# Performance work log

Measured on AMD Instinct MI355X. Metric: run time of the kernel, lower is better.

The kernel has to match this reference:

```python
import jax, jax.numpy as jnp
import numpy as np

B, T, E, H = 2, 2048, 1024, 4
Dk = E // H          # 256 head qk dim
Dv = Dk * 2          # 512 head v dim (expansion_ratio=2)
EPS = 1e-5
ROPE_BASE = 10000.0


def setup_inputs() -> dict:
    key = jax.random.key(0)
    ks = jax.random.split(key, 7)
    s = 0.02  # small init matching xavier gains in reset_parameters
    return {
        "x": jax.random.normal(ks[0], (B, T, E), jnp.float32),
        "Wq": jax.random.normal(ks[1], (E, E), jnp.float32) * s,
        "Wk": jax.random.normal(ks[2], (E, E), jnp.float32) * s,
        "Wv": jax.random.normal(ks[3], (E, 2 * E), jnp.float32) * s,
        "Wg": jax.random.normal(ks[4], (E, 2 * E), jnp.float32) * s,
        "Wo": jax.random.normal(ks[5], (2 * E, E), jnp.float32) * s,
        "gn_weight": jnp.ones((Dv,), jnp.float32),
    }


def _rotary(q, k):
    # q,k: [b, t, h, d]; non-interleaved (GPT-NeoX) rotary over the full head dim
    d = q.shape[-1]
    inv_freq = 1.0 / (ROPE_BASE ** (jnp.arange(0, d, 2, dtype=jnp.float32) / d))
    t = jnp.arange(q.shape[1], dtype=jnp.float32)
    freqs = jnp.einsum('t,f->tf', t, inv_freq)      # [t, d/2]
    cos = jnp.cos(freqs)[None, :, None, :]
    sin = jnp.sin(freqs)[None, :, None, :]

    def rot(x):
        x1, x2 = x[..., : d // 2], x[..., d // 2:]
        return jnp.concatenate([x1 * cos - x2 * sin, x2 * cos + x1 * sin], axis=-1)

    return rot(q), rot(k)


def reference(x, Wq, Wk, Wv, Wg, Wo, gn_weight):
    b, t, e = x.shape
    q = (x @ Wq).reshape(b, t, H, Dk)
    k = (x @ Wk).reshape(b, t, H, Dk)
    q, k = _rotary(q, k)
    q = q.transpose(0, 2, 1, 3) * (Dk ** -0.5)      # [b,h,t,dk], scale = head_qk_dim^-0.5
    k = k.transpose(0, 2, 1, 3)
    v = (x @ Wv).reshape(b, t, H, Dv).transpose(0, 2, 1, 3)  # [b,h,t,dv]

    # RetNet per-head decay: gamma_h = 1 - 2^-(5+h)
    gamma = 1.0 - jnp.exp2(-5.0 - jnp.arange(H, dtype=jnp.float32))
    ti = jnp.arange(t)
    n = ti[:, None] - ti[None, :]                   # t - s
    decay = jnp.where(
        n >= 0,
        gamma[:, None, None] ** jnp.maximum(n, 0).astype(jnp.float32),
        0.0,
    )                                               # [h,t,t] causal decayed mask

    scores = jnp.einsum('bhtd,bhsd->bhts', q, k) * decay[None]
    o = jnp.einsum('bhts,bhsd->bhtd', scores, v)    # [b,h,t,dv]
    o = o.transpose(0, 2, 1, 3)                     # [b,t,h,dv]

    # per-head RMSNorm (group_norm over head_v_dim)
    rms = jnp.sqrt(jnp.mean(o * o, axis=-1, keepdims=True) + EPS)
    o = o / rms * gn_weight

    # NOTE: the given source multiplies by raw g_proj(x) (gate_fn not applied in forward)
    g = x @ Wg                                      # [b,t,2E]
    return (o.reshape(b, t, H * Dv) * g) @ Wo       # [b,t,E]
```

## Files before the change

kernel.cpp:

```cpp
#include <hip/hip_runtime.h>
#include <hip/hip_bf16.h>

#define B_ 2
#define T_ 2048
#define E_ 1024
#define DK 256
#define DV 512
#define MROWS 4096
#define LDQKVG 6144
#define CHK 128
#define NCHK 16

typedef __attribute__((ext_vector_type(8))) short short8;
typedef __attribute__((ext_vector_type(4))) short short4v;
typedef __attribute__((ext_vector_type(4))) float floatx4;

typedef __attribute__((address_space(3))) unsigned as3_u32;
typedef const __attribute__((address_space(1))) unsigned as1_u32;

static __device__ __forceinline__ void gld_lds16(const unsigned short* gsrc, unsigned short* ldst) {
  __builtin_amdgcn_global_load_lds((as1_u32*)gsrc, (as3_u32*)ldst, 16, 0, 0);
}

static __device__ __forceinline__ float bf2f(unsigned short u) {
  union { unsigned int i; float f; } x; x.i = ((unsigned int)u) << 16; return x.f;
}
static __device__ __forceinline__ unsigned short f2bf(float f) {
  __hip_bfloat16 h = __float2bfloat16(f);
  return __builtin_bit_cast(unsigned short, h);
}

__global__ void __launch_bounds__(256) prep_kernel(
    const float* __restrict__ x, unsigned short* __restrict__ xb,
    const float* __restrict__ Wq, const float* __restrict__ Wk,
    const float* __restrict__ Wv, const float* __restrict__ Wg,
    unsigned short* __restrict__ WallT,
    const float* __restrict__ Wo, unsigned short* __restrict__ WoT,
    float2* __restrict__ ropetab) {
  __shared__ float tile[32][33];
  int bid = blockIdx.x;
  int tid = threadIdx.x;
  if (bid < 2048) {
    int i = bid * 256 + tid;
    size_t base = (size_t)i * 8;
    float4 a = *(const float4*)(x + base);
    float4 b = *(const float4*)(x + base + 4);
    short8 o;
    o[0] = (short)f2bf(a.x); o[1] = (short)f2bf(a.y);
    o[2] = (short)f2bf(a.z); o[3] = (short)f2bf(a.w);
    o[4] = (short)f2bf(b.x); o[5] = (short)f2bf(b.y);
    o[6] = (short)f2bf(b.z); o[7] = (short)f2bf(b.w);
    *(short8*)(xb + base) = o;
    return;
  }
  if (bid < 8192) {
    bid -= 2048;
    const float* in; unsigned short* o; int ldin, nbx;
    if (bid < 1024)      { in = Wq; o = WallT;                       ldin = 1024; nbx = 32; }
    else if (bid < 2048) { in = Wk; o = WallT + (size_t)1024 * 1024; ldin = 1024; nbx = 32; bid -= 1024; }
    else if (bid < 4096) { in = Wv; o = WallT + (size_t)2048 * 1024; ldin = 2048; nbx = 64; bid -= 2048; }
    else                 { in = Wg; o = WallT + (size_t)4096 * 1024; ldin = 2048; nbx = 64; bid -= 4096; }
    int c0 = (bid % nbx) * 32, r0 = (bid / nbx) * 32;
    int tx = tid & 31, ty = tid >> 5;
#pragma unroll
    for (int i = 0; i < 32; i += 8)
      tile[ty + i][tx] = in[(size_t)(r0 + ty + i) * ldin + c0 + tx];
    __syncthreads();
#pragma unroll
    for (int i = 0; i < 32; i += 8)
      o[(size_t)(c0 + ty + i) * 1024 + r0 + tx] = f2bf(tile[tx][ty + i]);
    return;
  }
  if (bid < 9216) {
    int idx = (bid - 8192) * 256 + tid;
    int t = idx >> 7, j = idx & 127;
    float invf = exp2f(-(float)j * (13.287712379549449f / 128.0f));
    float ang = (float)t * invf;
    ropetab[idx] = make_float2(cosf(ang), sinf(ang));
    return;
  }
  {
    int lb = bid - 9216;
    int c0 = (lb & 31) * 32, r0 = (lb >> 5) * 32;
    int tx = tid & 31, ty = tid >> 5;
#pragma unroll
    for (int i = 0; i < 32; i += 8)
      tile[ty + i][tx] = Wo[(size_t)(r0 + ty + i) * 1024 + c0 + tx];
    __syncthreads();
#pragma unroll
    for (int i = 0; i < 32; i += 8)
      WoT[(size_t)(c0 + ty + i) * 2048 + r0 + tx] = f2bf(tile[tx][ty + i]);
  }
}

template<int BM, int BN, int WM_W, int WN_W, int MINW, bool F32OUT>
__global__ void __launch_bounds__(WM_W * WN_W * 64, MINW) gemmp_kernel(
    const unsigned short* __restrict__ A, int lda,
    const unsigned short* __restrict__ Bt, int ldb, int K,
    void* __restrict__ Cp, int ldc, int ccol0, int nbx) {
  constexpr int WAVES = WM_W * WN_W;
  constexpr int AG = BM / 16 / WAVES;
  constexpr int BG = BN / 16 / WAVES;
  constexpr int RM = BM / WM_W;
  constexpr int CN = BN / WN_W;
  constexpr int MB = RM / 16, NB = CN / 16;
  __shared__ __align__(16) unsigned short lds[3][(BM + BN) * 32];
  const int tid = threadIdx.x;
  const int lane = tid & 63;
  const int wid = tid >> 6;
  const int wm = wid / WN_W, wn = wid % WN_W;
  const int bid = blockIdx.x;
  const int m0 = (bid % nbx) * BM;
  const int n0 = (bid / nbx) * BN;
  const unsigned short* Ab = A + (size_t)m0 * lda;
  const unsigned short* Bb = Bt + (size_t)n0 * ldb;
  const int NT = K / 32;

  auto stage = [&](int sl, int t) {
    const int k0 = t * 32;
#pragma unroll
    for (int j = 0; j < AG; ++j) {
      int g = wid * AG + j;
      int ci = g * 64 + lane;
      int row = ci >> 2, c = ci & 3;
      int cs = c ^ ((row >> 1) & 3);
      gld_lds16(Ab + (size_t)row * lda + k0 + cs * 8, &lds[sl][g * 512]);
    }
#pragma unroll
    for (int j = 0; j < BG; ++j) {
      int g = wid * BG + j;
      int ci = g * 64 + lane;
      int row = ci >> 2, c = ci & 3;
      int cs = c ^ ((row >> 1) & 3);
      gld_lds16(Bb + (size_t)row * ldb + k0 + cs * 8, &lds[sl][BM * 32 + g * 512]);
    }
  };

  floatx4 acc[MB][NB];
#pragma unroll
  for (int i = 0; i < MB; i++)
#pragma unroll
    for (int j = 0; j < NB; j++)
      acc[i][j] = (floatx4){0.f, 0.f, 0.f, 0.f};

  stage(0, 0);
  stage(1, 1);

  int cur = 0;
#pragma unroll 1
  for (int t = 0; t < NT; ++t) {
    if (t + 1 < NT) {
      if constexpr (AG + BG == 2) asm volatile("s_waitcnt vmcnt(2)" ::: "memory");
      else if constexpr (AG + BG == 3) asm volatile("s_waitcnt vmcnt(3)" ::: "memory");
      else if constexpr (AG + BG == 4) asm volatile("s_waitcnt vmcnt(4)" ::: "memory");
      else if constexpr (AG + BG == 6) asm volatile("s_waitcnt vmcnt(6)" ::: "memory");
      else asm volatile("s_waitcnt vmcnt(8)" ::: "memory");
    } else {
      asm volatile("s_waitcnt vmcnt(0)" ::: "memory");
    }
    __builtin_amdgcn_s_barrier();
    asm volatile("" ::: "memory");
    int sl = cur + 2; if (sl >= 3) sl -= 3;
    if (t + 2 < NT) stage(sl, t + 2);

    const unsigned short* As_ = lds[cur];
    const unsigned short* Bs_ = lds[cur] + BM * 32;
    short8 af[MB], bfv[NB];
#pragma unroll
    for (int i = 0; i < MB; ++i) {
      int row = wm * RM + i * 16 + (lane & 15);
      af[i] = *(const short8*)&As_[row * 32 + (((lane >> 4) ^ ((row >> 1) & 3)) * 8)];
    }
#pragma unroll
    for (int j = 0; j < NB; ++j) {
      int nn = wn * CN + j * 16 + (lane & 15);
      bfv[j] = *(const short8*)&Bs_[nn * 32 + (((lane >> 4) ^ ((nn >> 1) & 3)) * 8)];
    }
#pragma unroll
    for (int i = 0; i < MB; ++i)
#pragma unroll
      for (int j = 0; j < NB; ++j)
        acc[i][j] = __builtin_amdgcn_mfma_f32_16x16x32_bf16(af[i], bfv[j], acc[i][j], 0, 0, 0);
    cur = cur + 1 == 3 ? 0 : cur + 1;
  }

#pragma unroll
  for (int i = 0; i < MB; ++i)
#pragma unroll
    for (int j = 0; j < NB; ++j)
#pragma unroll
      for (int r = 0; r < 4; ++r) {
        int row = m0 + wm * RM + i * 16 + (lane >> 4) * 4 + r;
        int col = ccol0 + n0 + wn * CN + j * 16 + (lane & 15);
        float v = acc[i][j][r];
        if (F32OUT) ((float*)Cp)[(size_t)row * ldc + col] = v;
        else ((unsigned short*)Cp)[(size_t)row * ldc + col] = f2bf(v);
      }
}

__global__ void __launch_bounds__(256) postproc_kernel(
    unsigned short* __restrict__ qkvg, const float2* __restrict__ tab,
    unsigned short* __restrict__ kTs, unsigned short* __restrict__ vT) {
  __shared__ unsigned short kt[256][33];
  __shared__ unsigned short vt[512][33];
  const int tid = threadIdx.x;
  const int rt = blockIdx.x >> 2, h = blockIdx.x & 3;
  const int grow0 = rt * 32;
  const float lg = log2f(1.0f - exp2f(-5.0f - (float)h));
  const int r = tid >> 3;
  const int grow = grow0 + r;
  const int t = grow & (T_ - 1);
  const float sq = 0.0625f * exp2f((float)(t & (CHK - 1)) * lg);
  const float fac = exp2f((float)(CHK - (t & (CHK - 1))) * lg);
#pragma unroll
  for (int half = 0; half < 2; ++half) {
    int j0 = (tid & 7) * 8 + half * 64;
    size_t base = (size_t)grow * LDQKVG + h * DK + j0;
    short8 q1 = *(const short8*)&qkvg[base],      q2 = *(const short8*)&qkvg[base + 128];
    short8 k1 = *(const short8*)&qkvg[base + E_], k2 = *(const short8*)&qkvg[base + E_ + 128];
    short8 oq1, oq2, ok1, ok2;
#pragma unroll
    for (int e = 0; e < 8; ++e) {
      float2 cs = tab[(t << 7) + j0 + e];
      float c = cs.x, s = cs.y;
      float a1 = bf2f((unsigned short)q1[e]), a2 = bf2f((unsigned short)q2[e]);
      float b1 = bf2f((unsigned short)k1[e]), b2 = bf2f((unsigned short)k2[e]);
      float rk1 = b1 * c - b2 * s, rk2 = b2 * c + b1 * s;
      oq1[e] = (short)f2bf((a1 * c - a2 * s) * sq);
      oq2[e] = (short)f2bf((a2 * c + a1 * s) * sq);
      ok1[e] = (short)f2bf(rk1);
      ok2[e] = (short)f2bf(rk2);
      kt[j0 + e][r]       = f2bf(rk1 * fac);
      kt[j0 + e + 128][r] = f2bf(rk2 * fac);
    }
    *(short8*)&qkvg[base]            = oq1;
    *(short8*)&qkvg[base + 128]      = oq2;
    *(short8*)&qkvg[base + E_]       = ok1;
    *(short8*)&qkvg[base + E_ + 128] = ok2;
  }
  __syncthreads();
  {
    int dk = tid;
    unsigned short* dst = kTs + (size_t)(h * DK + dk) * MROWS + grow0;
#pragma unroll
    for (int i = 0; i < 4; ++i) {
      short8 w;
#pragma unroll
      for (int e = 0; e < 8; ++e) w[e] = (short)kt[dk][i * 8 + e];
      *(short8*)(dst + i * 8) = w;
    }
  }
  {
    int cv = tid & 7;
#pragma unroll
    for (int i = 0; i < 8; ++i) {
      int col = cv * 64 + i * 8;
      short8 v = *(const short8*)&qkvg[(size_t)grow * LDQKVG + 2048 + h * DV + col];
#pragma unroll
      for (int e = 0; e < 8; ++e) vt[col + e][r] = (unsigned short)v[e];
    }
  }
  __syncthreads();
#pragma unroll
  for (int p = 0; p < 2; ++p) {
    int dv = p * 256 + tid;
    unsigned short* dst = vT + (size_t)(h * DV + dv) * MROWS + grow0;
#pragma unroll
    for (int i = 0; i < 4; ++i) {
      short8 w;
#pragma unroll
      for (int e = 0; e < 8; ++e) w[e] = (short)vt[dv][i * 8 + e];
      *(short8*)(dst + i * 8) = w;
    }
  }
}

__global__ void __launch_bounds__(256) state_kernel(
    const unsigned short* __restrict__ kTs, const unsigned short* __restrict__ vT,
    unsigned short* __restrict__ Sbuf) {
  const int lane = threadIdx.x & 63, wid = threadIdx.x >> 6;
  const int bh = blockIdx.x & 7, dkt = (blockIdx.x >> 3) & 3, dvt = (blockIdx.x >> 5) & 15;
  const int b = bh >> 2, h = bh & 3;
  const float lg = log2f(1.0f - exp2f(-5.0f - (float)h));
  const float g128 = exp2f((float)CHK * lg);
  const int dk0 = dkt * 64 + wid * 16;
  const int dv0 = dvt * 32;
  const unsigned short* arow = kTs + (size_t)(h * DK + dk0 + (lane & 15)) * MROWS + b * T_ + (lane >> 4) * 8;
  const unsigned short* brow = vT + (size_t)(h * DV + dv0 + (lane & 15)) * MROWS + b * T_ + (lane >> 4) * 8;
  floatx4 acc[2];
  acc[0] = (floatx4){0.f, 0.f, 0.f, 0.f};
  acc[1] = (floatx4){0.f, 0.f, 0.f, 0.f};
#pragma unroll 4
  for (int c = 0; c < NCHK; ++c) {
    size_t sb = (size_t)(c * 8 + bh) * (DV * DK);
#pragma unroll
    for (int nb = 0; nb < 2; ++nb) {
      short4v o;
#pragma unroll
      for (int r = 0; r < 4; ++r) o[r] = (short)f2bf(acc[nb][r]);
      *(short4v*)&Sbuf[sb + (size_t)(dv0 + nb * 16 + (lane & 15)) * DK + dk0 + (lane >> 4) * 4] = o;
    }
#pragma unroll
    for (int nb = 0; nb < 2; ++nb)
#pragma unroll
      for (int r = 0; r < 4; ++r) acc[nb][r] *= g128;
#pragma unroll
    for (int ks = 0; ks < 4; ++ks) {
      short8 a = *(const short8*)(arow + c * CHK + ks * 32);
#pragma unroll
      for (int nb = 0; nb < 2; ++nb) {
        short8 bb = *(const short8*)(brow + (size_t)nb * 16 * MROWS + c * CHK + ks * 32);
        acc[nb] = __builtin_amdgcn_mfma_f32_16x16x32_bf16(a, bb, acc[nb], 0, 0, 0);
      }
    }
  }
}

__global__ void __launch_bounds__(256) retention3_kernel(
    const unsigned short* __restrict__ qkvg, const unsigned short* __restrict__ vT,
    const unsigned short* __restrict__ Sbuf, const float* __restrict__ gnw,
    unsigned short* __restrict__ og) {
  __shared__ unsigned short k_lds[32 * 256];
  __shared__ unsigned short v_lds[512 * 32];
  __shared__ unsigned short s_lds[4][16 * 40];
  const int tid = threadIdx.x, lane = tid & 63, wid = tid >> 6;
  const int bh  = blockIdx.x & 7;
  const int c   = (blockIdx.x >> 3) & 15;
  const int rhf = (blockIdx.x >> 7) & 1;
  const int b = bh >> 2, h = bh & 3;
  const float lg = log2f(1.0f - exp2f(-5.0f - (float)h));
  const int rb0 = b * T_ + c * CHK + rhf * 64;
  const int taub = rhf * 64 + wid * 16;
  const int nst = rhf ? 4 : 2;
  const unsigned short* kbase = qkvg + (size_t)(b * T_ + c * CHK) * LDQKVG + E_ + h * DK;
  const unsigned short* vbase = vT + (size_t)(h * DV) * MROWS + b * T_ + c * CHK;
  const unsigned short* Sp = Sbuf + (size_t)(c * 8 + bh) * (DV * DK);

  auto stage = [&](int st) {
    int s0 = st * 32;
#pragma unroll
    for (int j = 0; j < 4; ++j) {
      int ci = (wid * 4 + j) * 64 + lane;
      int row = ci >> 5, cc = ci & 31;
      int cs = cc ^ (row & 7);
      gld_lds16(kbase + (size_t)(s0 + row) * LDQKVG + cs * 8, &k_lds[(wid * 4 + j) * 512]);
    }
#pragma unroll
    for (int j = 0; j < 8; ++j) {
      int ci = (wid * 8 + j) * 64 + lane;
      int dv = ci >> 2, cc = ci & 3;
      int cs = cc ^ ((dv ^ (dv >> 2)) & 3);
      gld_lds16(vbase + (size_t)dv * MROWS + s0 + cs * 8, &v_lds[(wid * 8 + j) * 512]);
    }
  };

  stage(0);

  short8 qf[8];
  {
    int qrow = rb0 + wid * 16 + (lane & 15);
    const unsigned short* qp = qkvg + (size_t)qrow * LDQKVG + h * DK + (lane >> 4) * 8;
#pragma unroll
    for (int kk = 0; kk < 8; kk++) qf[kk] = *(const short8*)(qp + kk * 32);
  }
  floatx4 oacc[32];
#pragma unroll
  for (int nb = 0; nb < 32; ++nb) oacc[nb] = (floatx4){0.f, 0.f, 0.f, 0.f};
#pragma unroll
  for (int ks = 0; ks < 8; ++ks) {
#pragma unroll
    for (int nb = 0; nb < 32; ++nb) {
      short8 sf = *(const short8*)&Sp[(size_t)(nb * 16 + (lane & 15)) * DK + ks * 32 + (lane >> 4) * 8];
      oacc[nb] = __builtin_amdgcn_mfma_f32_16x16x32_bf16(qf[ks], sf, oacc[nb], 0, 0, 0);
    }
  }

#pragma unroll 1
  for (int st = 0; st < nst; ++st) {
    __syncthreads();
#pragma unroll
    for (int ch = 0; ch < 2; ++ch) {
      floatx4 f = (floatx4){0.f, 0.f, 0.f, 0.f};
      const int srow = ch * 16 + (lane & 15);
      __builtin_amdgcn_s_setprio(1);
#pragma unroll
      for (int kk = 0; kk < 8; kk++) {
        int cc = (kk * 4 + (lane >> 4)) ^ (srow & 7);
        short8 kf = *(const short8*)&k_lds[srow * 256 + cc * 8];
        f = __builtin_amdgcn_mfma_f32_16x16x32_bf16(qf[kk], kf, f, 0, 0, 0);
      }
      __builtin_amdgcn_s_setprio(0);
#pragma unroll
      for (int r = 0; r < 4; ++r) {
        int lr = (lane >> 4) * 4 + r;
        int sig = st * 32 + ch * 16 + (lane & 15);
        int n = taub + lr - sig;
        float val = (n >= 0) ? f[r] * exp2f(-(float)sig * lg) : 0.0f;
        s_lds[wid][lr * 40 + ch * 16 + (lane & 15)] = f2bf(val);
      }
    }
    short8 af = *(const short8*)&s_lds[wid][(lane & 15) * 40 + (lane >> 4) * 8];
    __builtin_amdgcn_s_setprio(1);
#pragma unroll
    for (int nb = 0; nb < 32; ++nb) {
      int dv = nb * 16 + (lane & 15);
      int cc = (lane >> 4) ^ ((dv ^ (dv >> 2)) & 3);
      short8 vf = *(const short8*)&v_lds[dv * 32 + cc * 8];
      oacc[nb] = __builtin_amdgcn_mfma_f32_16x16x32_bf16(af, vf, oacc[nb], 0, 0, 0);
    }
    __builtin_amdgcn_s_setprio(0);
    if (st + 1 < nst) {
      __syncthreads();
      stage(st + 1);
    }
  }
#pragma unroll
  for (int r = 0; r < 4; ++r) {
    float ss = 0.f;
#pragma unroll
    for (int nb = 0; nb < 32; nb++) { float xv = oacc[nb][r]; ss += xv * xv; }
    ss += __shfl_xor(ss, 1, 64);
    ss += __shfl_xor(ss, 2, 64);
    ss += __shfl_xor(ss, 4, 64);
    ss += __shfl_xor(ss, 8, 64);
    float inv = rsqrtf(ss * (1.0f / 512.0f) + 1e-5f);
    int row = rb0 + wid * 16 + (lane >> 4) * 4 + r;
    size_t growbase = (size_t)row * LDQKVG + 4096 + h * DV;
    size_t orowbase = (size_t)row * LDQKVG + h * DV;
#pragma unroll
    for (int nb = 0; nb < 32; nb++) {
      int col = nb * 16 + (lane & 15);
      float gv = bf2f(qkvg[growbase + col]);
      og[orowbase + col] = f2bf(oacc[nb][r] * inv * gnw[col] * gv);
    }
  }
}

extern "C" void kernel_launch(void* const* d_in, const int* in_sizes, int n_in,
                              void* d_out, int out_size, void* d_ws, size_t ws_size,
                              hipStream_t stream) {
  const float* x   = (const float*)d_in[0];
  const float* Wq  = (const float*)d_in[1];
  const float* Wk  = (const float*)d_in[2];
  const float* Wv  = (const float*)d_in[3];
  const float* Wg  = (const float*)d_in[4];
  const float* Wo  = (const float*)d_in[5];
  const float* gnw = (const float*)d_in[6];
  float* out = (float*)d_out;

  char* ws = (char*)d_ws;
  size_t off = 0;
  auto alloc = [&](size_t bytes) { char* p = ws + off; off += (bytes + 255) & ~(size_t)255; return p; };
  unsigned short* qkvg = (unsigned short*)alloc((size_t)MROWS * LDQKVG * 2);
  unsigned short* vT   = (unsigned short*)alloc((size_t)2048 * MROWS * 2);
  char* regS = alloc((size_t)NCHK * 8 * DV * DK * 2);
  unsigned short* Sbuf  = (unsigned short*)regS;
  unsigned short* xb    = (unsigned short*)regS;
  unsigned short* WallT = (unsigned short*)(regS + 8388608);
  unsigned short* kTs = (unsigned short*)alloc((size_t)1024 * MROWS * 2);
  unsigned short* WoT = (unsigned short*)alloc((size_t)1024 * 2048 * 2);
  float2* ropetab = (float2*)alloc((size_t)T_ * 128 * 8);
  unsigned short* og = qkvg + 2048;

  prep_kernel<<<11264, 256, 0, stream>>>(x, xb, Wq, Wk, Wv, Wg, WallT, Wo, WoT, ropetab);

  gemmp_kernel<128, 256, 2, 4, 4, false><<<768, 512, 0, stream>>>(
      xb, 1024, WallT, 1024, 1024, qkvg, LDQKVG, 0, 32);

  postproc_kernel<<<512, 256, 0, stream>>>(qkvg, ropetab, kTs, vT);

  state_kernel<<<512, 256, 0, stream>>>(kTs, vT, Sbuf);

  retention3_kernel<<<256, 256, 0, stream>>>(qkvg, vT, Sbuf, gnw, og);

  gemmp_kernel<128, 128, 2, 2, 3, true><<<256, 256, 0, stream>>>(
      og, LDQKVG, WoT, 2048, 2048, out, E_, 0, 32);
}
```

Before: 211.6 us.

## Add 256x256 double-buffered MFMA GEMM for the fused QKVG projection

Replaces the 128x256 triple-buffered GEMM used for the x·[Wq|Wk|Wv|Wg] projection with a new kernel. The new kernel uses 256x256 tiles, a K-step of 64 and a double-buffered LDS pipeline fed by direct global-to-LDS loads with an XOR swizzle. Each wave computes a 128x64 sub-tile and register-prefetches the A fragments, raising MFMA density and operand reuse per LDS byte. The larger tile halves the grid to 384 blocks and uses 128KB of LDS per block, which lowers occupancy and may leave fewer blocks per CU than the 256 CUs need for good load balance.

```diff
diff --git a/kernel.cpp b/kernel.cpp
--- a/kernel.cpp
+++ b/kernel.cpp
@@ -93,6 +93,110 @@
   }
 }
 
+template<int NBX>
+__global__ void __launch_bounds__(512, 2) gemm8_kernel(
+    const unsigned short* __restrict__ A, int lda,
+    const unsigned short* __restrict__ Bt, int ldb, int K,
+    unsigned short* __restrict__ Cp, int ldc) {
+  __shared__ __align__(16) unsigned short lds[2][2][256 * 64];
+  const int tid = threadIdx.x;
+  const int lane = tid & 63;
+  const int wid = tid >> 6;
+  const int wm = wid >> 2, wn = wid & 3;
+  const int m0 = (blockIdx.x % NBX) * 256;
+  const int n0 = (blockIdx.x / NBX) * 256;
+  const unsigned short* Ab = A + (size_t)m0 * lda;
+  const unsigned short* Bb = Bt + (size_t)n0 * ldb;
+  const int NT = K / 64;
+
+  auto stage = [&](int sl, int t) {
+    const int k0 = t * 64;
+#pragma unroll
+    for (int j = 0; j < 8; ++j) {
+      int cb = j * 512 + wid * 64;
+      int ci = cb + lane;
+      int arr = cb >> 11;
+      int ci2 = ci & 2047;
+      int row = ci2 >> 3, c16 = ci2 & 7;
+      int cs = c16 ^ (row & 7);
+      const unsigned short* src = (arr == 0)
+          ? Ab + (size_t)row * lda + k0 + cs * 8
+          : Bb + (size_t)row * ldb + k0 + cs * 8;
+      gld_lds16(src, &lds[sl][arr][(cb & 2047) * 8]);
+    }
+  };
+
+  floatx4 acc[8][4];
+#pragma unroll
+  for (int f = 0; f < 8; ++f)
+#pragma unroll
+    for (int g = 0; g < 4; ++g)
+      acc[f][g] = (floatx4){0.f, 0.f, 0.f, 0.f};
+
+  stage(0, 0);
+  stage(1, 1);
+
+  int cur = 0;
+#pragma unroll 1
+  for (int t = 0; t < NT; ++t) {
+    if (t + 1 < NT) asm volatile("s_waitcnt vmcnt(8)" ::: "memory");
+    else            asm volatile("s_waitcnt vmcnt(0)" ::: "memory");
+    __builtin_amdgcn_s_barrier();
+    asm volatile("" ::: "memory");
+
+    const unsigned short* Al = lds[cur][0];
+    const unsigned short* Bl = lds[cur][1];
+    auto rdA = [&](int f, int s) -> short8 {
+      int row = wm * 128 + f * 16 + (lane & 15);
+      int c16 = s * 4 + (lane >> 4);
+      return *(const short8*)&Al[row * 64 + ((c16 ^ (row & 7)) * 8)];
+    };
+    auto rdB = [&](int g, int s) -> short8 {
+      int row = wn * 64 + g * 16 + (lane & 15);
+      int c16 = s * 4 + (lane >> 4);
+      return *(const short8*)&Bl[row * 64 + ((c16 ^ (row & 7)) * 8)];
+    };
+
+    short8 bfr[4][2];
+#pragma unroll
+    for (int g = 0; g < 4; ++g) { bfr[g][0] = rdB(g, 0); bfr[g][1] = rdB(g, 1); }
+    short8 afA0 = rdA(0, 0), afA1 = rdA(0, 1);
+    short8 afB0, afB1;
+#pragma unroll
+    for (int f = 0; f < 8; ++f) {
+      if (f < 7) {
+        if (f & 1) { afA0 = rdA(f + 1, 0); afA1 = rdA(f + 1, 1); }
+        else       { afB0 = rdA(f + 1, 0); afB1 = rdA(f + 1, 1); }
+      }
+      const short8 a0 = (f & 1) ? afB0 : afA0;
+      const short8 a1 = (f & 1) ? afB1 : afA1;
+      __builtin_amdgcn_s_setprio(1);
+#pragma unroll
+      for (int g = 0; g < 4; ++g) {
+        acc[f][g] = __builtin_amdgcn_mfma_f32_16x16x32_bf16(a0, bfr[g][0], acc[f][g], 0, 0, 0);
+        acc[f][g] = __builtin_amdgcn_mfma_f32_16x16x32_bf16(a1, bfr[g][1], acc[f][g], 0, 0, 0);
+      }
+      __builtin_amdgcn_s_setprio(0);
+    }
+    asm volatile("s_waitcnt lgkmcnt(0)" ::: "memory");
+    __builtin_amdgcn_s_barrier();
+    asm volatile("" ::: "memory");
+    if (t + 2 < NT) stage(cur, t + 2);
+    cur ^= 1;
+  }
+
+#pragma unroll
+  for (int f = 0; f < 8; ++f)
+#pragma unroll
+    for (int g = 0; g < 4; ++g)
+#pragma unroll
+      for (int r = 0; r < 4; ++r) {
+        int row = m0 + wm * 128 + f * 16 + (lane >> 4) * 4 + r;
+        int col = n0 + wn * 64 + g * 16 + (lane & 15);
+        Cp[(size_t)row * ldc + col] = f2bf(acc[f][g][r]);
+      }
+}
+
 template<int BM, int BN, int WM_W, int WN_W, int MINW, bool F32OUT>
 __global__ void __launch_bounds__(WM_W * WN_W * 64, MINW) gemmp_kernel(
     const unsigned short* __restrict__ A, int lda,
@@ -464,8 +568,7 @@
 
   prep_kernel<<<11264, 256, 0, stream>>>(x, xb, Wq, Wk, Wv, Wg, WallT, Wo, WoT, ropetab);
 
-  gemmp_kernel<128, 256, 2, 4, 4, false><<<768, 512, 0, stream>>>(
-      xb, 1024, WallT, 1024, 1024, qkvg, LDQKVG, 0, 32);
+  gemm8_kernel<16><<<384, 512, 0, stream>>>(xb, 1024, WallT, 1024, 1024, qkvg, LDQKVG);
 
   postproc_kernel<<<512, 256, 0, stream>>>(qkvg, ropetab, kTs, vT);
 
```

Result: slower. 222.4 us (+5.1%).
